# Performance work log

Hardware: AMD Instinct MI355X
Metric: run time of the kernel (lower is better)

Reference implementation:

```python
import jax, jax.numpy as jnp
import numpy as np

B, H, N, D, BD, K = 8, 8, 65536, 128, 64, 32


def _l2norm(x, eps=1e-12):
    n = jnp.linalg.norm(x, axis=-1, keepdims=True)
    return x / jnp.maximum(n, eps)


def _topk_sparse_softmax(sim, k):
    # softmax over the top-k entries per (b,h); zeros elsewhere (== masked_fill -inf softmax)
    vals, idx = jax.lax.top_k(sim, k)              # [B,H,k]
    wk = jax.nn.softmax(vals, axis=-1)
    b = jnp.arange(sim.shape[0])[:, None, None]
    h = jnp.arange(sim.shape[1])[None, :, None]
    return jnp.zeros_like(sim).at[b, h, idx].set(wk)  # [B,H,N]


def setup_inputs() -> dict:
    key = jax.random.key(0)
    ks = jax.random.split(key, 14)
    return {
        "memory": jax.random.normal(ks[0], (B, N, D), jnp.float32),
        "read_keys": jax.random.normal(ks[1], (B, H, D), jnp.float32),
        "write_keys": jax.random.normal(ks[2], (B, H, D), jnp.float32),
        "write_vals": jax.random.normal(ks[3], (B, H, D), jnp.float32),
        "erase": jax.random.uniform(ks[4], (B, H), jnp.float32),
        "add_gate": jax.random.uniform(ks[5], (B, H), jnp.float32),
        "beta_r": jax.random.uniform(ks[6], (B, H), jnp.float32),
        "beta_w": jax.random.uniform(ks[7], (B, H), jnp.float32),
        "W_b1": jax.random.normal(ks[8], (D, BD), jnp.float32) * 0.02,
        "b_b1": jnp.zeros((BD,), jnp.float32),
        "W_b2": jax.random.normal(ks[9], (BD, D), jnp.float32) * 0.02,
        "b_b2": jnp.zeros((D,), jnp.float32),
        "W_merge": jax.random.normal(ks[10], (H * D, D), jnp.float32) * 0.02,
        "b_merge": jnp.zeros((D,), jnp.float32),
        "ln_g": jnp.ones((D,), jnp.float32),
        "ln_b": jnp.zeros((D,), jnp.float32),
        "decay_gate": jnp.ones((N,), jnp.float32) * 0.99,
    }


def reference(memory, read_keys, write_keys, write_vals, erase, add_gate,
              beta_r, beta_w, W_b1, b_b1, W_b2, b_b2, W_merge, b_merge,
              ln_g, ln_b, decay_gate):
    # ---- write (erase/add with top-k addressing, head-mean, normalize, decay) ----
    cvals = jax.nn.gelu(write_vals @ W_b1 + b_b1, approximate=False) @ W_b2 + b_b2  # [B,H,D]
    sim_w = jnp.einsum('bhd,bnd->bhn', _l2norm(write_keys), _l2norm(memory)) * beta_w[..., None]
    ww = _topk_sparse_softmax(sim_w, K)                                # [B,H,N]
    # mean_h[mem*(1-w*e)] = mem*(1-mean_h(w*e));  mean_h[w*add*cvals] via einsum/H
    erase_mean = (ww * erase[..., None]).mean(axis=1)                  # [B,N]
    add_part = jnp.einsum('bhn,bhd->bnd', ww * add_gate[..., None], cvals) / H
    mem2 = memory * (1.0 - erase_mean)[..., None] + add_part
    mem2 = _l2norm(mem2 + 1e-8)
    mem2 = mem2 * jax.nn.sigmoid(decay_gate)[None, :, None]            # decay gate

    # ---- read (from updated memory) ----
    sim_r = jnp.einsum('bhd,bnd->bhn', _l2norm(read_keys), _l2norm(mem2)) * beta_r[..., None]
    wr = _topk_sparse_softmax(sim_r, K)
    rph = jnp.einsum('bhn,bnd->bhd', wr, mem2).reshape(mem2.shape[0], H * D)
    merged = rph @ W_merge + b_merge                                   # [B,D]
    mu = merged.mean(axis=-1, keepdims=True)
    var = jnp.mean((merged - mu) ** 2, axis=-1, keepdims=True)
    out = (merged - mu) / jnp.sqrt(var + 1e-5) * ln_g + ln_b           # LayerNorm
    return out
```

## Files before the change

kernel.cpp:

```cpp
#include <hip/hip_runtime.h>
#include <hip/hip_bf16.h>

#define BB   8
#define HH   8
#define NN   65536
#define DD   128
#define BDIM 64
#define KK   32


#define OFF_SIMW 0u
#define OFF_SIMR (OFF_SIMW + 4194304u)
#define OFF_NWK  (OFF_SIMR + 4194304u)
#define OFF_NRK  (OFF_NWK + 8192u)
#define OFF_CV   (OFF_NRK + 8192u)
#define OFF_WIDX (OFF_CV + 8192u)
#define OFF_WVAL (OFF_WIDX + 2048u)
#define OFF_RIDX (OFF_WVAL + 2048u)
#define OFF_RVAL (OFF_RIDX + 2048u)
#define OFF_M2U  (OFF_RVAL + 2048u)
#define OFF_RPH  (OFF_M2U + 262144u)
#define OFF_CANDW (OFF_RPH + 8192u)
#define OFF_CANDR (OFF_CANDW + 262144u)

__device__ __forceinline__ unsigned ordf(float f) {
  unsigned u = __float_as_uint(f);
  return (u & 0x80000000u) ? ~u : (u | 0x80000000u);
}
__device__ __forceinline__ float unordf(unsigned u) {
  return (u & 0x80000000u) ? __uint_as_float(u & 0x7fffffffu) : __uint_as_float(~u);
}

__device__ __forceinline__ float brsum128(float v, float* sred, int tid) {
  #pragma unroll
  for (int o = 32; o > 0; o >>= 1) v += __shfl_xor(v, o);
  __syncthreads();
  if ((tid & 63) == 0) sred[tid >> 6] = v;
  __syncthreads();
  return sred[0] + sred[1];
}

__global__ __launch_bounds__(128) void k1_setup(
    const float* __restrict__ wkeys, const float* __restrict__ rkeys,
    const float* __restrict__ wvals,
    const float* __restrict__ beta_r, const float* __restrict__ beta_w,
    const float* __restrict__ W_b1, const float* __restrict__ b_b1,
    const float* __restrict__ W_b2, const float* __restrict__ b_b2,
    float* __restrict__ nwk, float* __restrict__ nrk,
    float* __restrict__ cvals, float* __restrict__ rph) {
  int g = blockIdx.x;
  int d = threadIdx.x;
  __shared__ float sred[2];
  __shared__ float wv_s[DD];
  __shared__ float hid[BDIM];

  rph[g * DD + d] = 0.f;

  float wk = wkeys[g * DD + d];
  float rk = rkeys[g * DD + d];
  float wv = wvals[g * DD + d];
  wv_s[d] = wv;

  float s = brsum128(wk * wk, sred, d);
  nwk[g * DD + d] = wk / fmaxf(sqrtf(s), 1e-12f) * beta_w[g];
  s = brsum128(rk * rk, sred, d);
  nrk[g * DD + d] = rk / fmaxf(sqrtf(s), 1e-12f) * beta_r[g];

  __syncthreads();
  if (d < BDIM) {
    float a = b_b1[d];
    #pragma unroll 4
    for (int dd = 0; dd < DD; ++dd) a += wv_s[dd] * W_b1[dd * BDIM + d];
    hid[d] = a * 0.5f * (1.f + erff(a * 0.70710678118654752f));
  }
  __syncthreads();
  float c = b_b2[d];
  #pragma unroll 4
  for (int j = 0; j < BDIM; ++j) c += hid[j] * W_b2[j * DD + d];
  cvals[g * DD + d] = c;
}

__global__ __launch_bounds__(256) void k2_sims(
    const float* __restrict__ mem,
    const float* __restrict__ nwk, const float* __restrict__ nrk,
    float* __restrict__ simw, float* __restrict__ simr) {
  int blk = blockIdx.x;
  int b   = blk >> 8;
  int n   = ((blk & 255) << 8) + threadIdx.x;
  const float4* rowp = (const float4*)(mem + ((size_t)b * NN + n) * DD);

  float dw[HH] = {0,0,0,0,0,0,0,0};
  float dr[HH] = {0,0,0,0,0,0,0,0};
  float nw = 0.f, nr = 0.f;
  const float* kw = nwk + b * HH * DD;
  const float* kr = nrk + b * HH * DD;

  for (int g = 0; g < 4; ++g) {
    float4 q[8];
    #pragma unroll
    for (int i = 0; i < 8; ++i) q[i] = rowp[g * 8 + i];
    #pragma unroll
    for (int i = 0; i < 8; ++i) {
      float xs[4] = {q[i].x, q[i].y, q[i].z, q[i].w};
      #pragma unroll
      for (int e = 0; e < 4; ++e) {
        float xv = xs[e];
        float xr = xv + 1e-8f;
        nw += xv * xv;
        nr += xr * xr;
        int d = g * 32 + i * 4 + e;
        #pragma unroll
        for (int h = 0; h < HH; ++h) {
          dw[h] += xv * kw[h * DD + d];
          dr[h] += xr * kr[h * DD + d];
        }
      }
    }
  }
  float riw = 1.f / fmaxf(sqrtf(nw), 1e-12f);
  float rir = 1.f / fmaxf(sqrtf(nr), 1e-12f);
  #pragma unroll
  for (int h = 0; h < HH; ++h) {
    simw[(size_t)(b * HH + h) * NN + n] = dw[h] * riw;
    simr[(size_t)(b * HH + h) * NN + n] = dr[h] * rir;
  }
}

__global__ __launch_bounds__(256) void t_stage1(
    const float* __restrict__ sims, unsigned long long* __restrict__ cand) {
  int blk   = blockIdx.x;
  int g     = blk >> 4;
  int chunk = blk & 15;
  int tid   = threadIdx.x;
  int w     = tid >> 6;
  int lane  = tid & 63;
  __shared__ unsigned long long sel[4][KK];

  const float4* s4 = (const float4*)(sims + (size_t)g * NN + chunk * 4096 + w * 1024);
  unsigned long long keys[16];
  #pragma unroll
  for (int i = 0; i < 4; ++i) {
    float4 q = s4[i * 64 + lane];
    int base = chunk * 4096 + w * 1024 + (i * 64 + lane) * 4;
    float xs[4] = {q.x, q.y, q.z, q.w};
    #pragma unroll
    for (int e = 0; e < 4; ++e)
      keys[i * 4 + e] = ((unsigned long long)ordf(xs[e]) << 32)
                        | (unsigned)(~(unsigned)(base + e));
  }
  unsigned live = 0xFFFFu;
  for (int k = 0; k < KK; ++k) {
    unsigned long long lbest = 0ull; int lslot = -1;
    #pragma unroll
    for (int j = 0; j < 16; ++j)
      if (((live >> j) & 1u) && keys[j] > lbest) { lbest = keys[j]; lslot = j; }
    unsigned long long best = lbest;
    #pragma unroll
    for (int o = 32; o > 0; o >>= 1) {
      unsigned long long t = __shfl_xor(best, o);
      if (t > best) best = t;
    }
    if (lbest == best && lslot >= 0) live &= ~(1u << lslot);
    if (lane == 0) sel[w][k] = best;
  }
  __syncthreads();
  if (lane < KK)
    cand[(size_t)g * 2048 + (chunk * 4 + w) * KK + lane] = sel[w][lane];
}

__global__ __launch_bounds__(64) void t_stage2(
    const unsigned long long* __restrict__ cand,
    int* __restrict__ oidx, float* __restrict__ oval) {
  int g    = blockIdx.x;
  int lane = threadIdx.x;
  __shared__ unsigned long long sel[KK];

  unsigned long long keys[32];
  #pragma unroll
  for (int i = 0; i < 32; ++i) keys[i] = cand[(size_t)g * 2048 + i * 64 + lane];

  unsigned live = 0xFFFFFFFFu;
  for (int k = 0; k < KK; ++k) {
    unsigned long long lbest = 0ull; int lslot = -1;
    #pragma unroll
    for (int j = 0; j < 32; ++j)
      if (((live >> j) & 1u) && keys[j] > lbest) { lbest = keys[j]; lslot = j; }
    unsigned long long best = lbest;
    #pragma unroll
    for (int o = 32; o > 0; o >>= 1) {
      unsigned long long t = __shfl_xor(best, o);
      if (t > best) best = t;
    }
    if (lbest == best && lslot >= 0) live &= ~(1u << lslot);
    if (lane == 0) sel[k] = best;
  }
  __syncthreads();
  if (lane < KK) {
    unsigned long long kk = sel[lane];
    float v  = unordf((unsigned)(kk >> 32));
    int idx  = (int)~(unsigned)(kk & 0xffffffffu);
    float m0 = unordf((unsigned)(sel[0] >> 32));
    float e  = expf(v - m0);
    float ss = e;
    #pragma unroll
    for (int o = 16; o > 0; o >>= 1) ss += __shfl_xor(ss, o);
    oidx[g * KK + lane] = idx;
    oval[g * KK + lane] = e / ss;
  }
}

__global__ __launch_bounds__(128) void k4_write(
    const float* __restrict__ mem, const float* __restrict__ erase,
    const float* __restrict__ adg,
    const int* __restrict__ widx, const float* __restrict__ wval,
    const float* __restrict__ cvals, const float* __restrict__ nrk,
    float* __restrict__ mem2u, float* __restrict__ simr) {
  int b  = blockIdx.x >> 8;
  int sl = blockIdx.x & 255;
  int d  = threadIdx.x;
  __shared__ int   swi[256];
  __shared__ float swv[256];
  __shared__ float sred[2 * 9];

  swi[d]       = widx[b * 256 + d];
  swi[d + 128] = widx[b * 256 + d + 128];
  swv[d]       = wval[b * 256 + d];
  swv[d + 128] = wval[b * 256 + d + 128];
  __syncthreads();

  int n = swi[sl];
  for (int j = 0; j < sl; ++j) if (swi[j] == n) return;

  float E = 0.f, addd = 0.f;
  #pragma unroll
  for (int h = 0; h < HH; ++h) {
    float er = erase[b * HH + h];
    float ag = adg[b * HH + h];
    float aw = 0.f;
    #pragma unroll 4
    for (int k = 0; k < KK; ++k) {
      int j = h * KK + k;
      if (swi[j] == n) { float wv = swv[j]; E += wv * er; aw += wv; }
    }
    addd += aw * ag * cvals[(b * HH + h) * DD + d];
  }
  float mval = mem[((size_t)b * NN + n) * DD + d];
  float v = mval * (1.f - E * 0.125f) + addd * 0.125f + 1e-8f;

  float r[9];
  r[0] = v * v;
  #pragma unroll
  for (int h = 0; h < HH; ++h) r[1 + h] = nrk[(b * HH + h) * DD + d] * v;
  #pragma unroll
  for (int o = 32; o > 0; o >>= 1) {
    #pragma unroll
    for (int i = 0; i < 9; ++i) r[i] += __shfl_xor(r[i], o);
  }
  if ((d & 63) == 0) {
    int w = d >> 6;
    #pragma unroll
    for (int i = 0; i < 9; ++i) sred[w * 9 + i] = r[i];
  }
  __syncthreads();
  float S    = sred[0] + sred[9];
  float rinv = 1.f / fmaxf(sqrtf(S), 1e-12f);
  mem2u[(size_t)(b * 256 + sl) * DD + d] = v * rinv;
  if (d < HH) simr[(size_t)(b * HH + d) * NN + n] = (sred[1 + d] + sred[9 + 1 + d]) * rinv;
}

__global__ __launch_bounds__(128) void k6_gather(
    const float* __restrict__ mem, const float* __restrict__ decay,
    const int* __restrict__ widx, const int* __restrict__ ridx,
    const float* __restrict__ rval, const float* __restrict__ mem2u,
    float* __restrict__ rph) {
  int b   = blockIdx.x >> 8;
  int rem = blockIdx.x & 255;
  int d   = threadIdx.x;
  __shared__ int swi[256];
  __shared__ float sred[2];
  swi[d]       = widx[b * 256 + d];
  swi[d + 128] = widx[b * 256 + d + 128];
  __syncthreads();

  int n   = ridx[b * HH * KK + rem];
  float w = rval[b * HH * KK + rem];
  float sc = 1.f / (1.f + expf(-decay[n]));
  int slot = -1;
  for (int j = 0; j < 256; ++j) if (swi[j] == n) { slot = j; break; }
  float u;
  if (slot >= 0) {
    u = mem2u[(size_t)(b * 256 + slot) * DD + d];
  } else {
    float v = mem[((size_t)b * NN + n) * DD + d] + 1e-8f;
    float S = brsum128(v * v, sred, d);
    u = v / fmaxf(sqrtf(S), 1e-12f);
  }
  int h = rem >> 5;
  atomicAdd(&rph[(b * HH + h) * DD + d], w * sc * u);
}

__global__ __launch_bounds__(512) void k7_merge(
    const float* __restrict__ rph, const float* __restrict__ W_merge,
    const float* __restrict__ b_merge, const float* __restrict__ ln_g,
    const float* __restrict__ ln_b, float* __restrict__ out) {
  int b = blockIdx.x;
  int tid = threadIdx.x;
  int d = tid & 127;
  int p = tid >> 7;
  __shared__ float acc_s[4][DD];
  __shared__ float accf[DD];
  __shared__ float smu, svar;

  float a = 0.f;
  int j0 = p * 256;
  #pragma unroll 4
  for (int j = j0; j < j0 + 256; ++j)
    a += rph[b * HH * DD + j] * W_merge[j * DD + d];
  acc_s[p][d] = a;
  __syncthreads();
  if (tid < DD) accf[d] = b_merge[d] + acc_s[0][d] + acc_s[1][d] + acc_s[2][d] + acc_s[3][d];
  __syncthreads();
  if (tid < 64) {
    float x0 = accf[tid], x1 = accf[tid + 64];
    float s1 = x0 + x1, s2 = x0 * x0 + x1 * x1;
    #pragma unroll
    for (int o = 32; o > 0; o >>= 1) { s1 += __shfl_xor(s1, o); s2 += __shfl_xor(s2, o); }
    if (tid == 0) { smu = s1 * (1.f / DD); svar = s2 * (1.f / DD) - smu * smu; }
  }
  __syncthreads();
  if (tid < DD)
    out[b * DD + d] = (accf[d] - smu) * rsqrtf(svar + 1e-5f) * ln_g[d] + ln_b[d];
}

extern "C" void kernel_launch(void* const* d_in, const int* in_sizes, int n_in,
                              void* d_out, int out_size, void* d_ws, size_t ws_size,
                              hipStream_t stream) {
  const float* memory  = (const float*)d_in[0];
  const float* rkeys   = (const float*)d_in[1];
  const float* wkeys   = (const float*)d_in[2];
  const float* wvals   = (const float*)d_in[3];
  const float* erase   = (const float*)d_in[4];
  const float* adg     = (const float*)d_in[5];
  const float* beta_r  = (const float*)d_in[6];
  const float* beta_w  = (const float*)d_in[7];
  const float* W_b1    = (const float*)d_in[8];
  const float* b_b1    = (const float*)d_in[9];
  const float* W_b2    = (const float*)d_in[10];
  const float* b_b2    = (const float*)d_in[11];
  const float* W_merge = (const float*)d_in[12];
  const float* b_merge = (const float*)d_in[13];
  const float* ln_g    = (const float*)d_in[14];
  const float* ln_b    = (const float*)d_in[15];
  const float* decay   = (const float*)d_in[16];

  float* ws   = (float*)d_ws;
  float* simw = ws + OFF_SIMW;
  float* simr = ws + OFF_SIMR;
  float* nwk  = ws + OFF_NWK;
  float* nrk  = ws + OFF_NRK;
  float* cv   = ws + OFF_CV;
  int*   widx = (int*)(ws + OFF_WIDX);
  float* wval = ws + OFF_WVAL;
  int*   ridx = (int*)(ws + OFF_RIDX);
  float* rval = ws + OFF_RVAL;
  float* m2u  = ws + OFF_M2U;
  float* rph  = ws + OFF_RPH;
  unsigned long long* candw = (unsigned long long*)(ws + OFF_CANDW);
  unsigned long long* candr = (unsigned long long*)(ws + OFF_CANDR);

  hipLaunchKernelGGL(k1_setup, dim3(BB * HH), dim3(128), 0, stream,
                     wkeys, rkeys, wvals, beta_r, beta_w, W_b1, b_b1, W_b2, b_b2,
                     nwk, nrk, cv, rph);
  hipLaunchKernelGGL(k2_sims, dim3(BB * (NN / 256)), dim3(256), 0, stream,
                     memory, nwk, nrk, simw, simr);
  hipLaunchKernelGGL(t_stage1, dim3(BB * HH * 16), dim3(256), 0, stream, simw, candw);
  hipLaunchKernelGGL(t_stage2, dim3(BB * HH), dim3(64), 0, stream, candw, widx, wval);
  hipLaunchKernelGGL(k4_write, dim3(BB * 256), dim3(128), 0, stream,
                     memory, erase, adg, widx, wval, cv, nrk, m2u, simr);
  hipLaunchKernelGGL(t_stage1, dim3(BB * HH * 16), dim3(256), 0, stream, simr, candr);
  hipLaunchKernelGGL(t_stage2, dim3(BB * HH), dim3(64), 0, stream, candr, ridx, rval);
  hipLaunchKernelGGL(k6_gather, dim3(BB * 256), dim3(128), 0, stream,
                     memory, decay, widx, ridx, rval, m2u, rph);
  hipLaunchKernelGGL(k7_merge, dim3(BB), dim3(512), 0, stream,
                     rph, W_merge, b_merge, ln_g, ln_b, (float*)d_out);
}
```

Measured before the change: 693.8 us.

## Fuse all stages into one persistent kernel with software grid barriers

Replaces the nine separate kernel launches with a single persistent kernel of 512 blocks. The stages are separated by an atomic-counter grid barrier, and each block loops over several chunks of the former grids. This removes launch gaps and per-kernel ramp-up and tail costs. In exchange it adds barrier spin overhead and depends on all 512 blocks being co-resident; the barrier gives up after a spin limit, which risks silently wrong results. The similarity stage also drops from 2048 blocks to 512 blocks each processing four chunks, which may reduce memory-level parallelism.

Measured after the change: 1.713 ms. 147% more time.

```diff
diff --git a/kernel.cpp b/kernel.cpp
--- a/kernel.cpp
+++ b/kernel.cpp
@@ -1,5 +1,4 @@
 #include <hip/hip_runtime.h>
-#include <hip/hip_bf16.h>
 
 #define BB   8
 #define HH   8
@@ -7,6 +6,7 @@
 #define DD   128
 #define BDIM 64
 #define KK   32
+#define NBLK 512
 
 
 #define OFF_SIMW 0u
@@ -22,6 +22,17 @@
 #define OFF_RPH  (OFF_M2U + 262144u)
 #define OFF_CANDW (OFF_RPH + 8192u)
 #define OFF_CANDR (OFF_CANDW + 262144u)
+#define OFF_BAR  (OFF_CANDR + 262144u)
+
+struct MegaArgs {
+  const float *mem, *rkeys, *wkeys, *wvals, *erase, *adg, *beta_r, *beta_w,
+              *W_b1, *b_b1, *W_b2, *b_b2, *W_merge, *b_merge, *ln_g, *ln_b, *decay;
+  float *simw, *simr, *nwk, *nrk, *cvals;
+  int *widx; float *wval; int *ridx; float *rval;
+  float *m2u, *rph;
+  unsigned long long *candw, *candr;
+  unsigned *bar; float *out;
+};
 
 __device__ __forceinline__ unsigned ordf(float f) {
   unsigned u = __float_as_uint(f);
@@ -31,111 +42,43 @@
   return (u & 0x80000000u) ? __uint_as_float(u & 0x7fffffffu) : __uint_as_float(~u);
 }
 
-__device__ __forceinline__ float brsum128(float v, float* sred, int tid) {
+__device__ __forceinline__ void gsync(unsigned* bar) {
+  __syncthreads();
+  if (threadIdx.x == 0) {
+    __threadfence();
+    unsigned g = __hip_atomic_load(&bar[1], __ATOMIC_ACQUIRE, __HIP_MEMORY_SCOPE_AGENT);
+    unsigned t = __hip_atomic_fetch_add(&bar[0], 1u, __ATOMIC_ACQ_REL, __HIP_MEMORY_SCOPE_AGENT);
+    if (t == NBLK - 1) {
+      __hip_atomic_store(&bar[0], 0u, __ATOMIC_RELAXED, __HIP_MEMORY_SCOPE_AGENT);
+      __hip_atomic_fetch_add(&bar[1], 1u, __ATOMIC_RELEASE, __HIP_MEMORY_SCOPE_AGENT);
+    } else {
+      long spins = 0;
+      while (__hip_atomic_load(&bar[1], __ATOMIC_ACQUIRE, __HIP_MEMORY_SCOPE_AGENT) == g) {
+        __builtin_amdgcn_s_sleep(8);
+        if (++spins > (1L << 22)) break;
+      }
+    }
+    __threadfence();
+  }
+  __syncthreads();
+}
+
+__device__ __forceinline__ float brsum256(float v, float* sred4, int tid) {
   #pragma unroll
   for (int o = 32; o > 0; o >>= 1) v += __shfl_xor(v, o);
   __syncthreads();
-  if ((tid & 63) == 0) sred[tid >> 6] = v;
-  __syncthreads();
-  return sred[0] + sred[1];
-}
-
-__global__ __launch_bounds__(128) void k1_setup(
-    const float* __restrict__ wkeys, const float* __restrict__ rkeys,
-    const float* __restrict__ wvals,
-    const float* __restrict__ beta_r, const float* __restrict__ beta_w,
-    const float* __restrict__ W_b1, const float* __restrict__ b_b1,
-    const float* __restrict__ W_b2, const float* __restrict__ b_b2,
-    float* __restrict__ nwk, float* __restrict__ nrk,
-    float* __restrict__ cvals, float* __restrict__ rph) {
-  int g = blockIdx.x;
-  int d = threadIdx.x;
-  __shared__ float sred[2];
-  __shared__ float wv_s[DD];
-  __shared__ float hid[BDIM];
-
-  rph[g * DD + d] = 0.f;
-
-  float wk = wkeys[g * DD + d];
-  float rk = rkeys[g * DD + d];
-  float wv = wvals[g * DD + d];
-  wv_s[d] = wv;
-
-  float s = brsum128(wk * wk, sred, d);
-  nwk[g * DD + d] = wk / fmaxf(sqrtf(s), 1e-12f) * beta_w[g];
-  s = brsum128(rk * rk, sred, d);
-  nrk[g * DD + d] = rk / fmaxf(sqrtf(s), 1e-12f) * beta_r[g];
-
-  __syncthreads();
-  if (d < BDIM) {
-    float a = b_b1[d];
-    #pragma unroll 4
-    for (int dd = 0; dd < DD; ++dd) a += wv_s[dd] * W_b1[dd * BDIM + d];
-    hid[d] = a * 0.5f * (1.f + erff(a * 0.70710678118654752f));
-  }
-  __syncthreads();
-  float c = b_b2[d];
-  #pragma unroll 4
-  for (int j = 0; j < BDIM; ++j) c += hid[j] * W_b2[j * DD + d];
-  cvals[g * DD + d] = c;
-}
-
-__global__ __launch_bounds__(256) void k2_sims(
-    const float* __restrict__ mem,
-    const float* __restrict__ nwk, const float* __restrict__ nrk,
-    float* __restrict__ simw, float* __restrict__ simr) {
-  int blk = blockIdx.x;
-  int b   = blk >> 8;
-  int n   = ((blk & 255) << 8) + threadIdx.x;
-  const float4* rowp = (const float4*)(mem + ((size_t)b * NN + n) * DD);
-
-  float dw[HH] = {0,0,0,0,0,0,0,0};
-  float dr[HH] = {0,0,0,0,0,0,0,0};
-  float nw = 0.f, nr = 0.f;
-  const float* kw = nwk + b * HH * DD;
-  const float* kr = nrk + b * HH * DD;
-
-  for (int g = 0; g < 4; ++g) {
-    float4 q[8];
-    #pragma unroll
-    for (int i = 0; i < 8; ++i) q[i] = rowp[g * 8 + i];
-    #pragma unroll
-    for (int i = 0; i < 8; ++i) {
-      float xs[4] = {q[i].x, q[i].y, q[i].z, q[i].w};
-      #pragma unroll
-      for (int e = 0; e < 4; ++e) {
-        float xv = xs[e];
-        float xr = xv + 1e-8f;
-        nw += xv * xv;
-        nr += xr * xr;
-        int d = g * 32 + i * 4 + e;
-        #pragma unroll
-        for (int h = 0; h < HH; ++h) {
-          dw[h] += xv * kw[h * DD + d];
-          dr[h] += xr * kr[h * DD + d];
-        }
-      }
-    }
-  }
-  float riw = 1.f / fmaxf(sqrtf(nw), 1e-12f);
-  float rir = 1.f / fmaxf(sqrtf(nr), 1e-12f);
-  #pragma unroll
-  for (int h = 0; h < HH; ++h) {
-    simw[(size_t)(b * HH + h) * NN + n] = dw[h] * riw;
-    simr[(size_t)(b * HH + h) * NN + n] = dr[h] * rir;
-  }
-}
-
-__global__ __launch_bounds__(256) void t_stage1(
-    const float* __restrict__ sims, unsigned long long* __restrict__ cand) {
-  int blk   = blockIdx.x;
-  int g     = blk >> 4;
-  int chunk = blk & 15;
-  int tid   = threadIdx.x;
-  int w     = tid >> 6;
-  int lane  = tid & 63;
-  __shared__ unsigned long long sel[4][KK];
-
+  if ((tid & 63) == 0) sred4[tid >> 6] = v;
+  __syncthreads();
+  float r = sred4[0] + sred4[1] + sred4[2] + sred4[3];
+  __syncthreads();
+  return r;
+}
+
+__device__ __forceinline__ void stage1_span(const float* __restrict__ sims,
+                            unsigned long long* __restrict__ cand,
+                            int vb, int tid, unsigned long long* sel) {
+  int g = vb >> 4, chunk = vb & 15;
+  int w = tid >> 6, lane = tid & 63;
   const float4* s4 = (const float4*)(sims + (size_t)g * NN + chunk * 4096 + w * 1024);
   unsigned long long keys[16];
   #pragma unroll
@@ -161,24 +104,21 @@
       if (t > best) best = t;
     }
     if (lbest == best && lslot >= 0) live &= ~(1u << lslot);
-    if (lane == 0) sel[w][k] = best;
+    if (lane == 0) sel[w * KK + k] = best;
   }
   __syncthreads();
   if (lane < KK)
-    cand[(size_t)g * 2048 + (chunk * 4 + w) * KK + lane] = sel[w][lane];
-}
-
-__global__ __launch_bounds__(64) void t_stage2(
-    const unsigned long long* __restrict__ cand,
-    int* __restrict__ oidx, float* __restrict__ oval) {
-  int g    = blockIdx.x;
-  int lane = threadIdx.x;
-  __shared__ unsigned long long sel[KK];
-
+    cand[(size_t)g * 2048 + (chunk * 4 + w) * KK + lane] = sel[w * KK + lane];
+  __syncthreads();
+}
+
+__device__ __forceinline__ void stage2_slice(const unsigned long long* __restrict__ cand,
+                             int g, int* __restrict__ oidx, float* __restrict__ oval,
+                             int tid, unsigned long long* sel) {
+  int lane = tid & 63;
   unsigned long long keys[32];
   #pragma unroll
   for (int i = 0; i < 32; ++i) keys[i] = cand[(size_t)g * 2048 + i * 64 + lane];
-
   unsigned live = 0xFFFFFFFFu;
   for (int k = 0; k < KK; ++k) {
     unsigned long long lbest = 0ull; int lslot = -1;
@@ -192,11 +132,11 @@
       if (t > best) best = t;
     }
     if (lbest == best && lslot >= 0) live &= ~(1u << lslot);
-    if (lane == 0) sel[k] = best;
-  }
-  __syncthreads();
-  if (lane < KK) {
-    unsigned long long kk = sel[lane];
+    if (tid == 0) sel[k] = best;
+  }
+  __syncthreads();
+  if (tid < KK) {
+    unsigned long long kk = sel[tid];
     float v  = unordf((unsigned)(kk >> 32));
     int idx  = (int)~(unsigned)(kk & 0xffffffffu);
     float m0 = unordf((unsigned)(sel[0] >> 32));
@@ -204,183 +144,282 @@
     float ss = e;
     #pragma unroll
     for (int o = 16; o > 0; o >>= 1) ss += __shfl_xor(ss, o);
-    oidx[g * KK + lane] = idx;
-    oval[g * KK + lane] = e / ss;
-  }
-}
-
-__global__ __launch_bounds__(128) void k4_write(
-    const float* __restrict__ mem, const float* __restrict__ erase,
-    const float* __restrict__ adg,
-    const int* __restrict__ widx, const float* __restrict__ wval,
-    const float* __restrict__ cvals, const float* __restrict__ nrk,
-    float* __restrict__ mem2u, float* __restrict__ simr) {
-  int b  = blockIdx.x >> 8;
-  int sl = blockIdx.x & 255;
-  int d  = threadIdx.x;
-  __shared__ int   swi[256];
-  __shared__ float swv[256];
-  __shared__ float sred[2 * 9];
-
-  swi[d]       = widx[b * 256 + d];
-  swi[d + 128] = widx[b * 256 + d + 128];
-  swv[d]       = wval[b * 256 + d];
-  swv[d + 128] = wval[b * 256 + d + 128];
-  __syncthreads();
-
-  int n = swi[sl];
-  for (int j = 0; j < sl; ++j) if (swi[j] == n) return;
-
-  float E = 0.f, addd = 0.f;
-  #pragma unroll
-  for (int h = 0; h < HH; ++h) {
-    float er = erase[b * HH + h];
-    float ag = adg[b * HH + h];
-    float aw = 0.f;
+    oidx[g * KK + tid] = idx;
+    oval[g * KK + tid] = e / ss;
+  }
+  __syncthreads();
+}
+
+__global__ __launch_bounds__(256, 2) void mega(MegaArgs A) {
+  const int blk = blockIdx.x;
+  const int tid = threadIdx.x;
+  __shared__ __align__(16) unsigned char smem[4608];
+
+  if (blk < BB * HH) {
+    float* sred4 = (float*)smem;
+    float* wv_s  = (float*)(smem + 16);
+    float* hid   = (float*)(smem + 16 + 512);
+    int g = blk, d = tid & 127;
+    bool act = tid < 128;
+
+    if (act) A.rph[g * DD + d] = 0.f;
+    float wk = act ? A.wkeys[g * DD + d] : 0.f;
+    float rk = act ? A.rkeys[g * DD + d] : 0.f;
+    float wv = act ? A.wvals[g * DD + d] : 0.f;
+    if (act) wv_s[d] = wv;
+
+    float s = brsum256(wk * wk, sred4, tid);
+    if (act) A.nwk[g * DD + d] = wk / fmaxf(sqrtf(s), 1e-12f) * A.beta_w[g];
+    s = brsum256(rk * rk, sred4, tid);
+    if (act) A.nrk[g * DD + d] = rk / fmaxf(sqrtf(s), 1e-12f) * A.beta_r[g];
+
+    __syncthreads();
+    if (tid < BDIM) {
+      float a = A.b_b1[tid];
+      #pragma unroll 4
+      for (int dd = 0; dd < DD; ++dd) a += wv_s[dd] * A.W_b1[dd * BDIM + tid];
+      hid[tid] = a * 0.5f * (1.f + erff(a * 0.70710678118654752f));
+    }
+    __syncthreads();
+    if (act) {
+      float c = A.b_b2[d];
+      #pragma unroll 4
+      for (int j = 0; j < BDIM; ++j) c += hid[j] * A.W_b2[j * DD + d];
+      A.cvals[g * DD + d] = c;
+    }
+  }
+  gsync(A.bar);
+
+  {
+    int b = blk >> 6;
+    const float* kw = A.nwk + b * HH * DD;
+    const float* kr = A.nrk + b * HH * DD;
+    for (int r = 0; r < 4; ++r) {
+      int chunk = blk * 4 + r;
+      int n = ((chunk & 255) << 8) + tid;
+      const float4* rowp = (const float4*)(A.mem + ((size_t)b * NN + n) * DD);
+      float dw[HH] = {0,0,0,0,0,0,0,0};
+      float dr[HH] = {0,0,0,0,0,0,0,0};
+      float nw = 0.f, nr = 0.f;
+      for (int g = 0; g < 4; ++g) {
+        float4 q[8];
+        #pragma unroll
+        for (int i = 0; i < 8; ++i) q[i] = rowp[g * 8 + i];
+        #pragma unroll
+        for (int i = 0; i < 8; ++i) {
+          float xs[4] = {q[i].x, q[i].y, q[i].z, q[i].w};
+          #pragma unroll
+          for (int e = 0; e < 4; ++e) {
+            float xv = xs[e];
+            float xr = xv + 1e-8f;
+            nw += xv * xv;
+            nr += xr * xr;
+            int d = g * 32 + i * 4 + e;
+            #pragma unroll
+            for (int h = 0; h < HH; ++h) {
+              dw[h] += xv * kw[h * DD + d];
+              dr[h] += xr * kr[h * DD + d];
+            }
+          }
+        }
+      }
+      float riw = 1.f / fmaxf(sqrtf(nw), 1e-12f);
+      float rir = 1.f / fmaxf(sqrtf(nr), 1e-12f);
+      #pragma unroll
+      for (int h = 0; h < HH; ++h) {
+        A.simw[(size_t)(b * HH + h) * NN + n] = dw[h] * riw;
+        A.simr[(size_t)(b * HH + h) * NN + n] = dr[h] * rir;
+      }
+    }
+  }
+  gsync(A.bar);
+
+  {
+    unsigned long long* sel = (unsigned long long*)smem;
+    stage1_span(A.simw, A.candw, blk * 2 + 0, tid, sel);
+    stage1_span(A.simw, A.candw, blk * 2 + 1, tid, sel);
+  }
+  gsync(A.bar);
+  if (blk < BB * HH)
+    stage2_slice(A.candw, blk, A.widx, A.wval, tid, (unsigned long long*)smem);
+  gsync(A.bar);
+
+  {
+    int b  = blk >> 6;
+    int s0 = (blk & 63) * 4;
+    int*   swi  = (int*)smem;
+    float* swv  = (float*)(smem + 1024);
+    float* sred = (float*)(smem + 2048);
+    swi[tid] = A.widx[b * 256 + tid];
+    swv[tid] = A.wval[b * 256 + tid];
+    __syncthreads();
+
+    int d = tid & 127;
+    bool act = tid < 128;
+    for (int q = 0; q < 4; ++q) {
+      int sl = s0 + q;
+      int n  = swi[sl];
+      bool dup = false;
+      for (int j = 0; j < sl; ++j) if (swi[j] == n) { dup = true; break; }
+      if (!dup) {
+        float E = 0.f, addd = 0.f;
+        #pragma unroll
+        for (int h = 0; h < HH; ++h) {
+          float er = A.erase[b * HH + h];
+          float ag = A.adg[b * HH + h];
+          float aw = 0.f;
+          #pragma unroll 4
+          for (int k = 0; k < KK; ++k) {
+            int j = h * KK + k;
+            if (swi[j] == n) { float wv = swv[j]; E += wv * er; aw += wv; }
+          }
+          addd += aw * ag * A.cvals[(b * HH + h) * DD + d];
+        }
+        float v = 0.f;
+        if (act) {
+          float mval = A.mem[((size_t)b * NN + n) * DD + d];
+          v = mval * (1.f - E * 0.125f) + addd * 0.125f + 1e-8f;
+        }
+        float r[9];
+        r[0] = v * v;
+        #pragma unroll
+        for (int h = 0; h < HH; ++h)
+          r[1 + h] = act ? A.nrk[(b * HH + h) * DD + d] * v : 0.f;
+        #pragma unroll
+        for (int o = 32; o > 0; o >>= 1) {
+          #pragma unroll
+          for (int i = 0; i < 9; ++i) r[i] += __shfl_xor(r[i], o);
+        }
+        if ((tid & 63) == 0) {
+          int w = tid >> 6;
+          #pragma unroll
+          for (int i = 0; i < 9; ++i) sred[w * 9 + i] = r[i];
+        }
+        __syncthreads();
+        float S    = sred[0] + sred[9] + sred[18] + sred[27];
+        float rinv = 1.f / fmaxf(sqrtf(S), 1e-12f);
+        if (act) A.m2u[(size_t)(b * 256 + sl) * DD + d] = v * rinv;
+        if (tid < HH) {
+          float p = sred[1 + tid] + sred[10 + tid] + sred[19 + tid] + sred[28 + tid];
+          A.simr[(size_t)(b * HH + tid) * NN + n] = p * rinv;
+        }
+      }
+      __syncthreads();
+    }
+  }
+  gsync(A.bar);
+
+  {
+    unsigned long long* sel = (unsigned long long*)smem;
+    stage1_span(A.simr, A.candr, blk * 2 + 0, tid, sel);
+    stage1_span(A.simr, A.candr, blk * 2 + 1, tid, sel);
+  }
+  gsync(A.bar);
+  if (blk < BB * HH)
+    stage2_slice(A.candr, blk, A.ridx, A.rval, tid, (unsigned long long*)smem);
+  gsync(A.bar);
+
+  {
+    int b  = blk >> 6;
+    int r0 = (blk & 63) * 4;
+    int*   swi   = (int*)smem;
+    float* sred4 = (float*)(smem + 1024);
+    swi[tid] = A.widx[b * 256 + tid];
+    __syncthreads();
+
+    int d = tid & 127;
+    bool act = tid < 128;
+    for (int q = 0; q < 4; ++q) {
+      int rem = r0 + q;
+      int n   = A.ridx[b * 256 + rem];
+      float w = A.rval[b * 256 + rem];
+      float sc = 1.f / (1.f + expf(-A.decay[n]));
+      int slot = -1;
+      for (int j = 0; j < 256; ++j) if (swi[j] == n) { slot = j; break; }
+      float u = 0.f;
+      if (slot >= 0) {
+        if (act) u = A.m2u[(size_t)(b * 256 + slot) * DD + d];
+      } else {
+        float v = act ? (A.mem[((size_t)b * NN + n) * DD + d] + 1e-8f) : 0.f;
+        float S = brsum256(v * v, sred4, tid);
+        u = v / fmaxf(sqrtf(S), 1e-12f);
+      }
+      int h = rem >> 5;
+      if (act) atomicAdd(&A.rph[(b * HH + h) * DD + d], w * sc * u);
+      __syncthreads();
+    }
+  }
+  gsync(A.bar);
+
+  if (blk < BB) {
+    int b = blk;
+    int d = tid & 127;
+    int p = tid >> 7;
+    float* acc_s = (float*)smem;
+    float* accf  = (float*)(smem + 1024);
+    float* stat  = (float*)(smem + 1536);
+
+    float a = 0.f;
+    int j0 = p * 512;
     #pragma unroll 4
-    for (int k = 0; k < KK; ++k) {
-      int j = h * KK + k;
-      if (swi[j] == n) { float wv = swv[j]; E += wv * er; aw += wv; }
-    }
-    addd += aw * ag * cvals[(b * HH + h) * DD + d];
-  }
-  float mval = mem[((size_t)b * NN + n) * DD + d];
-  float v = mval * (1.f - E * 0.125f) + addd * 0.125f + 1e-8f;
-
-  float r[9];
-  r[0] = v * v;
-  #pragma unroll
-  for (int h = 0; h < HH; ++h) r[1 + h] = nrk[(b * HH + h) * DD + d] * v;
-  #pragma unroll
-  for (int o = 32; o > 0; o >>= 1) {
-    #pragma unroll
-    for (int i = 0; i < 9; ++i) r[i] += __shfl_xor(r[i], o);
-  }
-  if ((d & 63) == 0) {
-    int w = d >> 6;
-    #pragma unroll
-    for (int i = 0; i < 9; ++i) sred[w * 9 + i] = r[i];
-  }
-  __syncthreads();
-  float S    = sred[0] + sred[9];
-  float rinv = 1.f / fmaxf(sqrtf(S), 1e-12f);
-  mem2u[(size_t)(b * 256 + sl) * DD + d] = v * rinv;
-  if (d < HH) simr[(size_t)(b * HH + d) * NN + n] = (sred[1 + d] + sred[9 + 1 + d]) * rinv;
-}
-
-__global__ __launch_bounds__(128) void k6_gather(
-    const float* __restrict__ mem, const float* __restrict__ decay,
-    const int* __restrict__ widx, const int* __restrict__ ridx,
-    const float* __restrict__ rval, const float* __restrict__ mem2u,
-    float* __restrict__ rph) {
-  int b   = blockIdx.x >> 8;
-  int rem = blockIdx.x & 255;
-  int d   = threadIdx.x;
-  __shared__ int swi[256];
-  __shared__ float sred[2];
-  swi[d]       = widx[b * 256 + d];
-  swi[d + 128] = widx[b * 256 + d + 128];
-  __syncthreads();
-
-  int n   = ridx[b * HH * KK + rem];
-  float w = rval[b * HH * KK + rem];
-  float sc = 1.f / (1.f + expf(-decay[n]));
-  int slot = -1;
-  for (int j = 0; j < 256; ++j) if (swi[j] == n) { slot = j; break; }
-  float u;
-  if (slot >= 0) {
-    u = mem2u[(size_t)(b * 256 + slot) * DD + d];
-  } else {
-    float v = mem[((size_t)b * NN + n) * DD + d] + 1e-8f;
-    float S = brsum128(v * v, sred, d);
-    u = v / fmaxf(sqrtf(S), 1e-12f);
-  }
-  int h = rem >> 5;
-  atomicAdd(&rph[(b * HH + h) * DD + d], w * sc * u);
-}
-
-__global__ __launch_bounds__(512) void k7_merge(
-    const float* __restrict__ rph, const float* __restrict__ W_merge,
-    const float* __restrict__ b_merge, const float* __restrict__ ln_g,
-    const float* __restrict__ ln_b, float* __restrict__ out) {
-  int b = blockIdx.x;
-  int tid = threadIdx.x;
-  int d = tid & 127;
-  int p = tid >> 7;
-  __shared__ float acc_s[4][DD];
-  __shared__ float accf[DD];
-  __shared__ float smu, svar;
-
-  float a = 0.f;
-  int j0 = p * 256;
-  #pragma unroll 4
-  for (int j = j0; j < j0 + 256; ++j)
-    a += rph[b * HH * DD + j] * W_merge[j * DD + d];
-  acc_s[p][d] = a;
-  __syncthreads();
-  if (tid < DD) accf[d] = b_merge[d] + acc_s[0][d] + acc_s[1][d] + acc_s[2][d] + acc_s[3][d];
-  __syncthreads();
-  if (tid < 64) {
-    float x0 = accf[tid], x1 = accf[tid + 64];
-    float s1 = x0 + x1, s2 = x0 * x0 + x1 * x1;
-    #pragma unroll
-    for (int o = 32; o > 0; o >>= 1) { s1 += __shfl_xor(s1, o); s2 += __shfl_xor(s2, o); }
-    if (tid == 0) { smu = s1 * (1.f / DD); svar = s2 * (1.f / DD) - smu * smu; }
-  }
-  __syncthreads();
-  if (tid < DD)
-    out[b * DD + d] = (accf[d] - smu) * rsqrtf(svar + 1e-5f) * ln_g[d] + ln_b[d];
+    for (int j = j0; j < j0 + 512; ++j)
+      a += A.rph[b * HH * DD + j] * A.W_merge[j * DD + d];
+    acc_s[p * DD + d] = a;
+    __syncthreads();
+    if (tid < DD) accf[d] = A.b_merge[d] + acc_s[d] + acc_s[DD + d];
+    __syncthreads();
+    if (tid < 64) {
+      float x0 = accf[tid], x1 = accf[tid + 64];
+      float s1 = x0 + x1, s2 = x0 * x0 + x1 * x1;
+      #pragma unroll
+      for (int o = 32; o > 0; o >>= 1) { s1 += __shfl_xor(s1, o); s2 += __shfl_xor(s2, o); }
+      if (tid == 0) { stat[0] = s1 * (1.f / DD); stat[1] = s2 * (1.f / DD) - stat[0] * stat[0]; }
+    }
+    __syncthreads();
+    if (tid < DD)
+      A.out[b * DD + d] = (accf[d] - stat[0]) * rsqrtf(stat[1] + 1e-5f) * A.ln_g[d] + A.ln_b[d];
+  }
 }
 
 extern "C" void kernel_launch(void* const* d_in, const int* in_sizes, int n_in,
                               void* d_out, int out_size, void* d_ws, size_t ws_size,
                               hipStream_t stream) {
-  const float* memory  = (const float*)d_in[0];
-  const float* rkeys   = (const float*)d_in[1];
-  const float* wkeys   = (const float*)d_in[2];
-  const float* wvals   = (const float*)d_in[3];
-  const float* erase   = (const float*)d_in[4];
-  const float* adg     = (const float*)d_in[5];
-  const float* beta_r  = (const float*)d_in[6];
-  const float* beta_w  = (const float*)d_in[7];
-  const float* W_b1    = (const float*)d_in[8];
-  const float* b_b1    = (const float*)d_in[9];
-  const float* W_b2    = (const float*)d_in[10];
-  const float* b_b2    = (const float*)d_in[11];
-  const float* W_merge = (const float*)d_in[12];
-  const float* b_merge = (const float*)d_in[13];
-  const float* ln_g    = (const float*)d_in[14];
-  const float* ln_b    = (const float*)d_in[15];
-  const float* decay   = (const float*)d_in[16];
-
-  float* ws   = (float*)d_ws;
-  float* simw = ws + OFF_SIMW;
-  float* simr = ws + OFF_SIMR;
-  float* nwk  = ws + OFF_NWK;
-  float* nrk  = ws + OFF_NRK;
-  float* cv   = ws + OFF_CV;
-  int*   widx = (int*)(ws + OFF_WIDX);
-  float* wval = ws + OFF_WVAL;
-  int*   ridx = (int*)(ws + OFF_RIDX);
-  float* rval = ws + OFF_RVAL;
-  float* m2u  = ws + OFF_M2U;
-  float* rph  = ws + OFF_RPH;
-  unsigned long long* candw = (unsigned long long*)(ws + OFF_CANDW);
-  unsigned long long* candr = (unsigned long long*)(ws + OFF_CANDR);
-
-  hipLaunchKernelGGL(k1_setup, dim3(BB * HH), dim3(128), 0, stream,
-                     wkeys, rkeys, wvals, beta_r, beta_w, W_b1, b_b1, W_b2, b_b2,
-                     nwk, nrk, cv, rph);
-  hipLaunchKernelGGL(k2_sims, dim3(BB * (NN / 256)), dim3(256), 0, stream,
-                     memory, nwk, nrk, simw, simr);
-  hipLaunchKernelGGL(t_stage1, dim3(BB * HH * 16), dim3(256), 0, stream, simw, candw);
-  hipLaunchKernelGGL(t_stage2, dim3(BB * HH), dim3(64), 0, stream, candw, widx, wval);
-  hipLaunchKernelGGL(k4_write, dim3(BB * 256), dim3(128), 0, stream,
-                     memory, erase, adg, widx, wval, cv, nrk, m2u, simr);
-  hipLaunchKernelGGL(t_stage1, dim3(BB * HH * 16), dim3(256), 0, stream, simr, candr);
-  hipLaunchKernelGGL(t_stage2, dim3(BB * HH), dim3(64), 0, stream, candr, ridx, rval);
-  hipLaunchKernelGGL(k6_gather, dim3(BB * 256), dim3(128), 0, stream,
-                     memory, decay, widx, ridx, rval, m2u, rph);
-  hipLaunchKernelGGL(k7_merge, dim3(BB), dim3(512), 0, stream,
-                     rph, W_merge, b_merge, ln_g, ln_b, (float*)d_out);
-}
+  float* ws = (float*)d_ws;
+
+  MegaArgs A;
+  A.mem     = (const float*)d_in[0];
+  A.rkeys   = (const float*)d_in[1];
+  A.wkeys   = (const float*)d_in[2];
+  A.wvals   = (const float*)d_in[3];
+  A.erase   = (const float*)d_in[4];
+  A.adg     = (const float*)d_in[5];
+  A.beta_r  = (const float*)d_in[6];
+  A.beta_w  = (const float*)d_in[7];
+  A.W_b1    = (const float*)d_in[8];
+  A.b_b1    = (const float*)d_in[9];
+  A.W_b2    = (const float*)d_in[10];
+  A.b_b2    = (const float*)d_in[11];
+  A.W_merge = (const float*)d_in[12];
+  A.b_merge = (const float*)d_in[13];
+  A.ln_g    = (const float*)d_in[14];
+  A.ln_b    = (const float*)d_in[15];
+  A.decay   = (const float*)d_in[16];
+  A.simw    = ws + OFF_SIMW;
+  A.simr    = ws + OFF_SIMR;
+  A.nwk     = ws + OFF_NWK;
+  A.nrk     = ws + OFF_NRK;
+  A.cvals   = ws + OFF_CV;
+  A.widx    = (int*)(ws + OFF_WIDX);
+  A.wval    = ws + OFF_WVAL;
+  A.ridx    = (int*)(ws + OFF_RIDX);
+  A.rval    = ws + OFF_RVAL;
+  A.m2u     = ws + OFF_M2U;
+  A.rph     = ws + OFF_RPH;
+  A.candw   = (unsigned long long*)(ws + OFF_CANDW);
+  A.candr   = (unsigned long long*)(ws + OFF_CANDR);
+  A.bar     = (unsigned*)(ws + OFF_BAR);
+  A.out     = (float*)d_out;
+
+  hipMemsetAsync((void*)A.bar, 0, 16, stream);
+  hipLaunchKernelGGL(mega, dim3(NBLK), dim3(256), 0, stream, A);
+}
```
